# Optimization experiments

Hardware: AMD Instinct MI355X
Metric: run time of the kernel (lower is better)

The kernel has to match this reference:

```python
import jax, jax.numpy as jnp
import numpy as np

B, N, H, W = 2, 2048, 256, 256
C = 128
STATE = 256
FEAT_IN = C + 2
MID = 6  # layer_num - 2 residual blocks
OUT_DIM = 2


def setup_inputs() -> dict:
    key = jax.random.key(0)
    ks = jax.random.split(key, 8)
    s = 0.01  # matches nn.Linear init normal_(0.0, 0.01)
    features = jax.random.normal(ks[0], (B, C, H, W), jnp.float32)
    base_point = jax.random.uniform(ks[1], (B, N, 2), dtype=jnp.float32)
    adj = jax.random.uniform(ks[2], (B, N, N), dtype=jnp.float32) / N  # row-normalized-ish adjacency
    point_mask = jnp.ones((B, 1, N, 1), jnp.float32)
    w_first = jax.random.normal(ks[3], (2, FEAT_IN, STATE), jnp.float32) * s  # fc1, fc2
    b_first = jnp.zeros((2, STATE), jnp.float32)
    w_mid = jax.random.normal(ks[4], (MID, 4, STATE, STATE), jnp.float32) * s  # per block: gcn1.fc1, gcn1.fc2, gcn2.fc1, gcn2.fc2
    b_mid = jnp.zeros((MID, 4, STATE), jnp.float32)
    w_last = jax.random.normal(ks[5], (2, STATE, STATE), jnp.float32) * s
    b_last = jnp.zeros((2, STATE), jnp.float32)
    w_fc = jax.random.normal(ks[6], (STATE, OUT_DIM), jnp.float32) * s
    b_fc = jnp.zeros((OUT_DIM,), jnp.float32)
    return dict(features=features, base_point=base_point, adj=adj, point_mask=point_mask,
                w_first=w_first, b_first=b_first, w_mid=w_mid, b_mid=b_mid,
                w_last=w_last, b_last=b_last, w_fc=w_fc, b_fc=b_fc)


def _interp(feat, coords, h, w):
    # feat: [B, H*W, C]; coords: [B, N, 2] in [0,1] (x, y order as in torch code)
    Xs = coords[:, :, 0] * w
    Ys = coords[:, :, 1] * h
    X0f = jnp.floor(Xs); X1f = X0f + 1.0
    Y0f = jnp.floor(Ys); Y1f = Y0f + 1.0
    w00 = (X1f - Xs) * (Y1f - Ys)
    w01 = (X1f - Xs) * (Ys - Y0f)
    w10 = (Xs - X0f) * (Y1f - Ys)
    w11 = (Xs - X0f) * (Ys - Y0f)
    X0 = jnp.clip(X0f, 0, w - 1).astype(jnp.int32)
    X1 = jnp.clip(X1f, 0, w - 1).astype(jnp.int32)
    Y0 = jnp.clip(Y0f, 0, h - 1).astype(jnp.int32)
    Y1 = jnp.clip(Y1f, 0, h - 1).astype(jnp.int32)
    def gather(idx):  # idx: [B, N] -> [B, N, C]
        return jnp.take_along_axis(feat, idx[:, :, None], axis=1)
    m00 = gather(X0 + Y0 * w)
    m01 = gather(X0 + Y1 * w)
    m10 = gather(X1 + Y0 * w)
    m11 = gather(X1 + Y1 * w)
    return (w00[..., None] * m00 + w01[..., None] * m01 +
            w10[..., None] * m10 + w11[..., None] * m11)


def _gconv(x, adj, w1, b1, w2, b2):
    # GraphConvolution: fc1(x) + fc2(adj @ x)
    return (x @ w1 + b1) + (jnp.matmul(adj, x) @ w2 + b2)


def _res_block(x, adj, w, b):
    h = jax.nn.relu(_gconv(x, adj, w[0], b[0], w[1], b[1]))
    h = _gconv(h, adj, w[2], b[2], w[3], b[3])
    return jax.nn.relu(h + x)


def _forward(features, base_point, adj, point_mask,
             w_first, b_first, w_mid, b_mid, w_last, b_last, w_fc, b_fc):
    b, c, h, w = features.shape
    feat_flat = features.reshape(b, c, h * w).transpose(0, 2, 1)  # [B, HW, C]
    cnn_feature = _interp(feat_flat, base_point, h, w)            # [B, N, C]
    x = jnp.concatenate([cnn_feature, base_point], axis=2)        # [B, N, C+2]
    x = _gconv(x, adj, w_first[0], b_first[0], w_first[1], b_first[1])
    for i in range(MID):
        x = _res_block(x, adj, w_mid[i], b_mid[i])
    x = _gconv(x, adj, w_last[0], b_last[0], w_last[1], b_last[1])
    gcn_pred = x @ w_fc + b_fc                                    # [B, N, out_dim]
    mask = point_mask.squeeze(1)                                  # [B, N, 1]
    pred_points = base_point + gcn_pred[:, :, :2] * mask
    lap1 = base_point - jnp.matmul(adj, base_point)
    lap2 = pred_points - jnp.matmul(adj, pred_points)
    lap_energy = jnp.sqrt((((lap2 - lap1) ** 2) + 1e-10).sum(-1)).mean(-1)  # [B]
    return pred_points, gcn_pred, lap_energy


def reference(features, base_point, adj, point_mask,
              w_first, b_first, w_mid, b_mid, w_last, b_last, w_fc, b_fc):
    return _forward(features, base_point, adj, point_mask,
                    w_first, b_first, w_mid, b_mid, w_last, b_last, w_fc, b_fc)
```

## Files before the change

### kernel.cpp

```cpp
#include <hip/hip_runtime.h>
#include <hip/hip_bf16.h>
#include <math.h>

#define BB 2
#define NN 2048
#define HH 256
#define WW 256
#define CC 128
#define MIDN 6
#define YSTR 1048576

typedef __hip_bfloat16 bf16;
typedef short short8 __attribute__((ext_vector_type(8)));
typedef float f32x4 __attribute__((ext_vector_type(4)));
typedef unsigned short ushort4v __attribute__((ext_vector_type(4)));

__device__ inline float bf2f(unsigned short u) {
    return __uint_as_float(((unsigned int)u) << 16);
}
__device__ inline unsigned short f2bf_bits(float f) {
    __hip_bfloat16 h = __float2bfloat16(f);
    return *reinterpret_cast<unsigned short*>(&h);
}

__global__ void prep_kernel(const float* __restrict__ adj, bf16* __restrict__ adjB,
                            const float* __restrict__ features, const float* __restrict__ base_point,
                            bf16* __restrict__ x0p,
                            const float* __restrict__ w_first, const float* __restrict__ w_mid,
                            const float* __restrict__ w_last, bf16* __restrict__ wT) {
    __shared__ float tbuf[32][33];
    int bid = blockIdx.x;
    int t = threadIdx.x;
    if (bid < 8192) {
        int sub = bid >> 1;
        if ((bid & 1) == 0) {
            size_t i = ((size_t)sub * 256 + t) * 8;
            float4 f0 = *(const float4*)(adj + i);
            float4 f1 = *(const float4*)(adj + i + 4);
            short8 v;
            v[0] = (short)f2bf_bits(f0.x); v[1] = (short)f2bf_bits(f0.y);
            v[2] = (short)f2bf_bits(f0.z); v[3] = (short)f2bf_bits(f0.w);
            v[4] = (short)f2bf_bits(f1.x); v[5] = (short)f2bf_bits(f1.y);
            v[6] = (short)f2bf_bits(f1.z); v[7] = (short)f2bf_bits(f1.w);
            *(short8*)(adjB + i) = v;
        } else {
            int idx = sub;
            int b   = idx >> 11;
            float xs = base_point[idx * 2 + 0] * (float)WW;
            float ys = base_point[idx * 2 + 1] * (float)HH;
            float x0f = floorf(xs), y0f = floorf(ys);
            float x1f = x0f + 1.f, y1f = y0f + 1.f;
            float w00 = (x1f - xs) * (y1f - ys);
            float w01 = (x1f - xs) * (ys - y0f);
            float w10 = (xs - x0f) * (y1f - ys);
            float w11 = (xs - x0f) * (ys - y0f);
            int X0 = (int)fminf(fmaxf(x0f, 0.f), (float)(WW - 1));
            int X1 = (int)fminf(fmaxf(x1f, 0.f), (float)(WW - 1));
            int Y0 = (int)fminf(fmaxf(y0f, 0.f), (float)(HH - 1));
            int Y1 = (int)fminf(fmaxf(y1f, 0.f), (float)(HH - 1));
            int p00 = Y0 * WW + X0, p01 = Y1 * WW + X0;
            int p10 = Y0 * WW + X1, p11 = Y1 * WW + X1;
            float val = 0.f;
            if (t < CC) {
                const float* f = features + (size_t)(b * CC + t) * (HH * WW);
                val = w00 * f[p00] + w01 * f[p01] + w10 * f[p10] + w11 * f[p11];
            } else if (t == CC) {
                val = base_point[idx * 2 + 0];
            } else if (t == CC + 1) {
                val = base_point[idx * 2 + 1];
            }
            x0p[(size_t)idx * 256 + t] = __float2bfloat16(val);
        }
    } else {
        int idx = bid - 8192;
        int m   = idx >> 6;
        int sub = idx & 63;
        int bx = sub & 7, by = sub >> 3;
        const float* S; int R;
        if (m < 2)       { S = w_first + (size_t)m * 130 * 256; R = 130; }
        else if (m < 26) { S = w_mid + (size_t)(m - 2) * 65536; R = 256; }
        else             { S = w_last + (size_t)(m - 26) * 65536; R = 256; }
        bf16* D = wT + (size_t)m * 65536;
        int tx = t & 31, ty = t >> 5;
        int c0 = bx * 32, r0 = by * 32;
        #pragma unroll
        for (int k = 0; k < 4; ++k) {
            int r = r0 + ty + 8 * k;
            tbuf[ty + 8 * k][tx] = (r < R) ? S[(size_t)r * 256 + c0 + tx] : 0.f;
        }
        __syncthreads();
        #pragma unroll
        for (int k = 0; k < 4; ++k) {
            int c = c0 + ty + 8 * k;
            D[(size_t)c * 256 + r0 + tx] = __float2bfloat16(tbuf[tx][ty + 8 * k]);
        }
    }
}

__global__ __launch_bounds__(256) void s_kernel(const bf16* __restrict__ gprev,
                                                const bf16* __restrict__ Yb,
                                                const float* __restrict__ bias1,
                                                const float* __restrict__ bias2,
                                                const bf16* __restrict__ res,
                                                int relu,
                                                const bf16* __restrict__ wcat,
                                                bf16* __restrict__ xR,
                                                bf16* __restrict__ g1out,
                                                bf16* __restrict__ g2T) {
    __shared__ bf16 Al[32 * 64];
    __shared__ bf16 Bl[128 * 64];
    int tid = threadIdx.x;
    int bid = blockIdx.x;
    int lin = (bid & 7) * 64 + (bid >> 3);
    int ct = lin & 3, rt = lin >> 2;
    int lane = tid & 63, w = tid >> 6;
    int wr = w >> 1, wc = w & 1;
    int row16 = lane & 15, kg = lane >> 4;
    f32x4 acc[4] = {};
    for (int it = 0; it < 4; ++it) {
        {
            int d = tid * 16;
            int row = d >> 7;
            int cb = d & 127;
            int gcol = it * 64 + (cb >> 1);
            int ridx = rt * 32 + row;
            size_t off = (size_t)ridx * 256 + gcol;
            short8 gv = *(const short8*)(gprev + off);
            short8 pk;
            if (Yb) {
                float fv[8];
                #pragma unroll
                for (int j = 0; j < 8; ++j) fv[j] = bf2f((unsigned short)gv[j]);
                #pragma unroll
                for (int p = 0; p < 4; ++p) {
                    short8 yv = *(const short8*)(Yb + (size_t)p * YSTR + off);
                    #pragma unroll
                    for (int j = 0; j < 8; ++j) fv[j] += bf2f((unsigned short)yv[j]);
                }
                short8 rv = {};
                if (res) rv = *(const short8*)(res + off);
                #pragma unroll
                for (int j = 0; j < 8; ++j) {
                    float f = fv[j] + bias1[gcol + j] + bias2[gcol + j];
                    if (res)  f += bf2f((unsigned short)rv[j]);
                    if (relu) f = fmaxf(f, 0.f);
                    pk[j] = (short)f2bf_bits(f);
                }
            } else {
                pk = gv;
            }
            if (ct == 0) *(short8*)(xR + off) = pk;
            int byte = row * 128 + (cb ^ ((row & 7) << 4));
            *(short8*)((char*)Al + byte) = pk;
        }
        #pragma unroll
        for (int rnd = 0; rnd < 4; ++rnd) {
            int d = tid * 16 + rnd * 4096;
            int row = d >> 7;
            int cb = d & 127;
            int sc = (cb ^ ((row & 7) << 4)) >> 1;
            __builtin_amdgcn_global_load_lds(
                (const __attribute__((address_space(1))) void*)(wcat + (size_t)(ct * 128 + row) * 256 + it * 64 + sc),
                (__attribute__((address_space(3))) void*)((char*)Bl + (w << 10) + rnd * 4096),
                16, 0, 0);
        }
        asm volatile("s_waitcnt vmcnt(0)" ::: "memory");
        __syncthreads();
        #pragma unroll
        for (int kk = 0; kk < 2; ++kk) {
            int arow = wr * 16 + row16;
            int abyte = arow * 128 + (((kk * 64) + kg * 16) ^ ((arow & 7) << 4));
            short8 a = *(const short8*)((const char*)Al + abyte);
            #pragma unroll
            for (int nf = 0; nf < 4; ++nf) {
                int fr = wc * 64 + nf * 16 + row16;
                int byte = fr * 128 + (((kk * 64) + kg * 16) ^ ((fr & 7) << 4));
                short8 bfr = *(const short8*)((const char*)Bl + byte);
                acc[nf] = __builtin_amdgcn_mfma_f32_16x16x32_bf16(a, bfr, acc[nf], 0, 0, 0);
            }
        }
        __syncthreads();
    }
    int cbase = ct * 128 + wc * 64;
    int rb = rt * 32 + wr * 16 + kg * 4;
    if (cbase < 256) {
        #pragma unroll
        for (int nf = 0; nf < 4; ++nf) {
            int c = cbase + nf * 16 + row16;
            #pragma unroll
            for (int j = 0; j < 4; ++j)
                *reinterpret_cast<unsigned short*>(&g1out[(size_t)(rb + j) * 256 + c]) = f2bf_bits(acc[nf][j]);
        }
    } else {
        #pragma unroll
        for (int nf = 0; nf < 4; ++nf) {
            int c = cbase - 256 + nf * 16 + row16;
            ushort4v pk;
            #pragma unroll
            for (int j = 0; j < 4; ++j) pk[j] = f2bf_bits(acc[nf][j]);
            *(ushort4v*)(g2T + (size_t)c * 4096 + rb) = pk;
        }
    }
}

__global__ __launch_bounds__(256) void adjb_kernel(const bf16* __restrict__ adjB,
                                                   const bf16* __restrict__ g2T,
                                                   bf16* __restrict__ Ybase) {
    __shared__ bf16 Al[128 * 64];
    __shared__ bf16 Bl[64 * 64];
    int tid = threadIdx.x;
    int bid = blockIdx.x;
    int lin = (bid & 7) * 64 + (bid >> 3);
    int ct = lin & 3, rt = (lin >> 2) & 15, z = lin >> 6;
    int b = z >> 2, ks = z & 3;
    const bf16* Aadj = adjB + (size_t)b * NN * NN + (size_t)(rt * 128) * NN + ks * 512;
    const bf16* Bg   = g2T + (size_t)(ct * 64) * 4096 + b * NN + ks * 512;
    bf16* Yo = Ybase + (size_t)ks * YSTR;
    int lane = tid & 63, w = tid >> 6;
    int wr = w >> 1, wc = w & 1;
    int row16 = lane & 15, kg = lane >> 4;
    f32x4 acc[4][2] = {};
    for (int it = 0; it < 8; ++it) {
        int k0 = it * 64;
        #pragma unroll
        for (int rnd = 0; rnd < 4; ++rnd) {
            int d = tid * 16 + rnd * 4096;
            int row = d >> 7, cb = d & 127;
            int sc = (cb ^ ((row & 7) << 4)) >> 1;
            __builtin_amdgcn_global_load_lds(
                (const __attribute__((address_space(1))) void*)(Aadj + (size_t)row * NN + k0 + sc),
                (__attribute__((address_space(3))) void*)((char*)Al + (w << 10) + rnd * 4096),
                16, 0, 0);
        }
        #pragma unroll
        for (int rnd = 0; rnd < 2; ++rnd) {
            int d = tid * 16 + rnd * 4096;
            int row = d >> 7, cb = d & 127;
            int sc = (cb ^ ((row & 7) << 4)) >> 1;
            __builtin_amdgcn_global_load_lds(
                (const __attribute__((address_space(1))) void*)(Bg + (size_t)row * 4096 + k0 + sc),
                (__attribute__((address_space(3))) void*)((char*)Bl + (w << 10) + rnd * 4096),
                16, 0, 0);
        }
        asm volatile("s_waitcnt vmcnt(0)" ::: "memory");
        __syncthreads();
        #pragma unroll
        for (int kk = 0; kk < 2; ++kk) {
            short8 a[4], bfr[2];
            #pragma unroll
            for (int mf = 0; mf < 4; ++mf) {
                int row = wr * 64 + mf * 16 + row16;
                int byte = row * 128 + (((kk * 64) + kg * 16) ^ ((row & 7) << 4));
                a[mf] = *(const short8*)((const char*)Al + byte);
            }
            #pragma unroll
            for (int nf = 0; nf < 2; ++nf) {
                int fr = wc * 32 + nf * 16 + row16;
                int byte = fr * 128 + (((kk * 64) + kg * 16) ^ ((fr & 7) << 4));
                bfr[nf] = *(const short8*)((const char*)Bl + byte);
            }
            #pragma unroll
            for (int mf = 0; mf < 4; ++mf)
                #pragma unroll
                for (int nf = 0; nf < 2; ++nf)
                    acc[mf][nf] = __builtin_amdgcn_mfma_f32_16x16x32_bf16(a[mf], bfr[nf], acc[mf][nf], 0, 0, 0);
        }
        __syncthreads();
    }
    #pragma unroll
    for (int mf = 0; mf < 4; ++mf) {
        #pragma unroll
        for (int nf = 0; nf < 2; ++nf) {
            int c  = ct * 64 + wc * 32 + nf * 16 + row16;
            int r0 = b * NN + rt * 128 + wr * 64 + mf * 16 + kg * 4;
            #pragma unroll
            for (int j = 0; j < 4; ++j)
                *reinterpret_cast<unsigned short*>(&Yo[(size_t)(r0 + j) * 256 + c]) = f2bf_bits(acc[mf][nf][j]);
        }
    }
}

__global__ void head_kernel(const bf16* __restrict__ g1, const bf16* __restrict__ Yb,
                            const float* __restrict__ b_last,
                            const float* __restrict__ w_fc, const float* __restrict__ b_fc,
                            const float* __restrict__ base_point, const float* __restrict__ point_mask,
                            float* __restrict__ out, float* __restrict__ dpts) {
    int row = blockIdx.x * 256 + threadIdx.x;
    float s0 = b_fc[0], s1 = b_fc[1];
    for (int d = 0; d < 256; d += 8) {
        size_t off = (size_t)row * 256 + d;
        short8 a = *(const short8*)(g1 + off);
        float zv[8];
        #pragma unroll
        for (int j = 0; j < 8; ++j) zv[j] = bf2f((unsigned short)a[j]);
        #pragma unroll
        for (int p = 0; p < 4; ++p) {
            short8 yv = *(const short8*)(Yb + (size_t)p * YSTR + off);
            #pragma unroll
            for (int j = 0; j < 8; ++j) zv[j] += bf2f((unsigned short)yv[j]);
        }
        #pragma unroll
        for (int j = 0; j < 8; ++j) {
            float z = zv[j] + b_last[d + j] + b_last[256 + d + j];
            s0 += z * w_fc[(d + j) * 2 + 0];
            s1 += z * w_fc[(d + j) * 2 + 1];
        }
    }
    float m  = point_mask[row];
    float p0 = base_point[row * 2 + 0] + s0 * m;
    float p1 = base_point[row * 2 + 1] + s1 * m;
    out[row * 2 + 0] = p0;
    out[row * 2 + 1] = p1;
    out[2 * BB * NN + row * 2 + 0] = s0;
    out[2 * BB * NN + row * 2 + 1] = s1;
    dpts[row * 2 + 0] = s0 * m;
    dpts[row * 2 + 1] = s1 * m;
}

__global__ void lap_rows(const bf16* __restrict__ adjB, const float* __restrict__ dpts,
                         float* __restrict__ tvals) {
    int w    = threadIdx.x >> 6;
    int lane = threadIdx.x & 63;
    int row  = blockIdx.x * 4 + w;
    int b = row >> 11, n = row & 2047;
    const bf16* ar = adjB + (size_t)b * NN * NN + (size_t)n * NN;
    const float* db = dpts + (size_t)b * NN * 2;
    float s0 = 0.f, s1 = 0.f;
    for (int k4 = 0; k4 < 4; ++k4) {
        int k = k4 * 512 + lane * 8;
        short8 av = *(const short8*)(ar + k);
        #pragma unroll
        for (int j = 0; j < 8; ++j) {
            float a = bf2f((unsigned short)av[j]);
            float2 dv = *(const float2*)(db + (k + j) * 2);
            s0 += a * dv.x;
            s1 += a * dv.y;
        }
    }
    for (int off = 32; off; off >>= 1) {
        s0 += __shfl_xor(s0, off);
        s1 += __shfl_xor(s1, off);
    }
    if (lane == 0) {
        float e0 = dpts[(size_t)row * 2 + 0] - s0;
        float e1 = dpts[(size_t)row * 2 + 1] - s1;
        tvals[row] = sqrtf(e0 * e0 + e1 * e1 + 1e-10f);
    }
}

__global__ void lap_reduce(const float* __restrict__ tvals, float* __restrict__ outp) {
    __shared__ float sd[256];
    int b = blockIdx.x;
    float s = 0.f;
    for (int i = threadIdx.x; i < NN; i += 256) s += tvals[b * NN + i];
    sd[threadIdx.x] = s;
    __syncthreads();
    for (int o = 128; o; o >>= 1) {
        if (threadIdx.x < o) sd[threadIdx.x] += sd[threadIdx.x + o];
        __syncthreads();
    }
    if (threadIdx.x == 0) outp[b] = sd[0] / (float)NN;
}

extern "C" void kernel_launch(void* const* d_in, const int* in_sizes, int n_in,
                              void* d_out, int out_size, void* d_ws, size_t ws_size,
                              hipStream_t stream) {
    const float* features   = (const float*)d_in[0];
    const float* base_point = (const float*)d_in[1];
    const float* adj        = (const float*)d_in[2];
    const float* point_mask = (const float*)d_in[3];
    const float* w_first    = (const float*)d_in[4];
    const float* b_first    = (const float*)d_in[5];
    const float* w_mid      = (const float*)d_in[6];
    const float* b_mid      = (const float*)d_in[7];
    const float* w_last     = (const float*)d_in[8];
    const float* b_last     = (const float*)d_in[9];
    const float* w_fc       = (const float*)d_in[10];
    const float* b_fc       = (const float*)d_in[11];
    float* out = (float*)d_out;
    char* W = (char*)d_ws;

    bf16* adjB   = (bf16*)W;
    bf16* wT     = (bf16*)(W + 16777216);
    bf16* x0p    = (bf16*)(W + 20447232);
    bf16* g1b[2] = { (bf16*)(W + 22544384), (bf16*)(W + 24641536) };
    bf16* g2T    = (bf16*)(W + 26738688);
    bf16* Yb     = (bf16*)(W + 28835840);
    bf16* xsl[2] = { (bf16*)(W + 37224448), (bf16*)(W + 39321600) };
    bf16* xscr   = (bf16*)(W + 41418752);
    float* dpts  = (float*)(W + 43515904);
    float* tvals = (float*)(W + 43548672);

    prep_kernel<<<9984, 256, 0, stream>>>(adj, adjB, features, base_point, x0p,
                                          w_first, w_mid, w_last, wT);

    s_kernel<<<512, 256, 0, stream>>>(x0p, nullptr, nullptr, nullptr, nullptr, 0,
                                      wT, xscr, g1b[0], g2T);
    adjb_kernel<<<512, 256, 0, stream>>>(adjB, g2T, Yb);

    for (int k = 1; k < 14; ++k) {
        const float *bb1, *bb2;
        const bf16* resp = nullptr;
        bf16* xw;
        int rl;
        if (k == 1) {
            bb1 = b_first; bb2 = b_first + 256; rl = 0; xw = xsl[0];
        } else if ((k & 1) == 0) {
            int m = (k - 2) / 2;
            bb1 = b_mid + (size_t)m * 1024; bb2 = bb1 + 256;
            rl = 1; xw = xscr;
        } else {
            int m = (k - 3) / 2;
            bb1 = b_mid + (size_t)m * 1024 + 512; bb2 = bb1 + 256;
            rl = 1;
            resp = xsl[m & 1];
            xw   = xsl[((k - 1) / 2) & 1];
        }
        s_kernel<<<512, 256, 0, stream>>>(g1b[(k - 1) & 1], Yb, bb1, bb2, resp, rl,
                                          wT + (size_t)2 * k * 65536, xw, g1b[k & 1], g2T);
        adjb_kernel<<<512, 256, 0, stream>>>(adjB, g2T, Yb);
    }

    head_kernel<<<16, 256, 0, stream>>>(g1b[1], Yb, b_last, w_fc, b_fc,
                                        base_point, point_mask, out, dpts);
    lap_rows<<<1024, 256, 0, stream>>>(adjB, dpts, tvals);
    lap_reduce<<<BB, 256, 0, stream>>>(tvals, out + 4 * BB * NN);
}
```

Measured before the change: 339.9 us.

## Double-buffer LDS tiles in s_kernel and adjb_kernel, restructure prep kernel blocks

Both GEMM kernels (s_kernel and adjb_kernel) now keep two LDS buffers, so the global loads for the next k-slice are issued before the MFMAs on the current slice run. This hides memory latency, and s_kernel also overlaps the A-operand elementwise combine (bias, residual, relu). The prep kernel is reorganised: interpolation uses one wave per point with two channels per lane, and the adj conversion does 16 elements per thread, which cuts the block count from 9984 to 4864. The cost is twice the LDS per block, which may lower occupancy, plus more live registers for the prefetched A values.

```diff
diff --git a/kernel.cpp b/kernel.cpp
--- a/kernel.cpp
+++ b/kernel.cpp
@@ -31,48 +31,53 @@
     __shared__ float tbuf[32][33];
     int bid = blockIdx.x;
     int t = threadIdx.x;
-    if (bid < 8192) {
-        int sub = bid >> 1;
-        if ((bid & 1) == 0) {
-            size_t i = ((size_t)sub * 256 + t) * 8;
-            float4 f0 = *(const float4*)(adj + i);
-            float4 f1 = *(const float4*)(adj + i + 4);
+    if (bid < 1024) {
+        int wv = t >> 6, lane = t & 63;
+        int idx = bid * 4 + wv;
+        int b   = idx >> 11;
+        float bx = base_point[idx * 2 + 0];
+        float by = base_point[idx * 2 + 1];
+        float xs = bx * (float)WW;
+        float ys = by * (float)HH;
+        float x0f = floorf(xs), y0f = floorf(ys);
+        float x1f = x0f + 1.f, y1f = y0f + 1.f;
+        float w00 = (x1f - xs) * (y1f - ys);
+        float w01 = (x1f - xs) * (ys - y0f);
+        float w10 = (xs - x0f) * (y1f - ys);
+        float w11 = (xs - x0f) * (ys - y0f);
+        int X0 = (int)fminf(fmaxf(x0f, 0.f), (float)(WW - 1));
+        int X1 = (int)fminf(fmaxf(x1f, 0.f), (float)(WW - 1));
+        int Y0 = (int)fminf(fmaxf(y0f, 0.f), (float)(HH - 1));
+        int Y1 = (int)fminf(fmaxf(y1f, 0.f), (float)(HH - 1));
+        int p00 = Y0 * WW + X0, p01 = Y1 * WW + X0;
+        int p10 = Y0 * WW + X1, p11 = Y1 * WW + X1;
+        int c0 = lane * 2;
+        const float* f0 = features + (size_t)(b * CC + c0) * (HH * WW);
+        const float* f1 = f0 + HH * WW;
+        float v0 = w00 * f0[p00] + w01 * f0[p01] + w10 * f0[p10] + w11 * f0[p11];
+        float v1 = w00 * f1[p00] + w01 * f1[p01] + w10 * f1[p10] + w11 * f1[p11];
+        unsigned int pk = (unsigned int)f2bf_bits(v0) | ((unsigned int)f2bf_bits(v1) << 16);
+        *(unsigned int*)(x0p + (size_t)idx * 256 + c0) = pk;
+        unsigned int pk2 = 0;
+        if (lane == 0)
+            pk2 = (unsigned int)f2bf_bits(bx) | ((unsigned int)f2bf_bits(by) << 16);
+        *(unsigned int*)(x0p + (size_t)idx * 256 + 128 + c0) = pk2;
+    } else if (bid < 3072) {
+        int sub = bid - 1024;
+        size_t i = ((size_t)sub * 4096) + (size_t)t * 16;
+        #pragma unroll
+        for (int h = 0; h < 2; ++h) {
+            float4 f0 = *(const float4*)(adj + i + h * 8);
+            float4 f1 = *(const float4*)(adj + i + h * 8 + 4);
             short8 v;
             v[0] = (short)f2bf_bits(f0.x); v[1] = (short)f2bf_bits(f0.y);
             v[2] = (short)f2bf_bits(f0.z); v[3] = (short)f2bf_bits(f0.w);
             v[4] = (short)f2bf_bits(f1.x); v[5] = (short)f2bf_bits(f1.y);
             v[6] = (short)f2bf_bits(f1.z); v[7] = (short)f2bf_bits(f1.w);
-            *(short8*)(adjB + i) = v;
-        } else {
-            int idx = sub;
-            int b   = idx >> 11;
-            float xs = base_point[idx * 2 + 0] * (float)WW;
-            float ys = base_point[idx * 2 + 1] * (float)HH;
-            float x0f = floorf(xs), y0f = floorf(ys);
-            float x1f = x0f + 1.f, y1f = y0f + 1.f;
-            float w00 = (x1f - xs) * (y1f - ys);
-            float w01 = (x1f - xs) * (ys - y0f);
-            float w10 = (xs - x0f) * (y1f - ys);
-            float w11 = (xs - x0f) * (ys - y0f);
-            int X0 = (int)fminf(fmaxf(x0f, 0.f), (float)(WW - 1));
-            int X1 = (int)fminf(fmaxf(x1f, 0.f), (float)(WW - 1));
-            int Y0 = (int)fminf(fmaxf(y0f, 0.f), (float)(HH - 1));
-            int Y1 = (int)fminf(fmaxf(y1f, 0.f), (float)(HH - 1));
-            int p00 = Y0 * WW + X0, p01 = Y1 * WW + X0;
-            int p10 = Y0 * WW + X1, p11 = Y1 * WW + X1;
-            float val = 0.f;
-            if (t < CC) {
-                const float* f = features + (size_t)(b * CC + t) * (HH * WW);
-                val = w00 * f[p00] + w01 * f[p01] + w10 * f[p10] + w11 * f[p11];
-            } else if (t == CC) {
-                val = base_point[idx * 2 + 0];
-            } else if (t == CC + 1) {
-                val = base_point[idx * 2 + 1];
-            }
-            x0p[(size_t)idx * 256 + t] = __float2bfloat16(val);
+            *(short8*)(adjB + i + h * 8) = v;
         }
     } else {
-        int idx = bid - 8192;
+        int idx = bid - 3072;
         int m   = idx >> 6;
         int sub = idx & 63;
         int bx = sub & 7, by = sub >> 3;
@@ -107,8 +112,8 @@
                                                 bf16* __restrict__ xR,
                                                 bf16* __restrict__ g1out,
                                                 bf16* __restrict__ g2T) {
-    __shared__ bf16 Al[32 * 64];
-    __shared__ bf16 Bl[128 * 64];
+    __shared__ bf16 Al[2 * 32 * 64];
+    __shared__ bf16 Bl[2 * 128 * 64];
     int tid = threadIdx.x;
     int bid = blockIdx.x;
     int lin = (bid & 7) * 64 + (bid >> 3);
@@ -116,71 +121,98 @@
     int lane = tid & 63, w = tid >> 6;
     int wr = w >> 1, wc = w & 1;
     int row16 = lane & 15, kg = lane >> 4;
+
+    int ad  = tid * 16;
+    int arw = ad >> 7;
+    int acb = ad & 127;
+    int ridx = rt * 32 + arw;
+    int awbyte = arw * 128 + (acb ^ ((arw & 7) << 4));
+    int gc_base = acb >> 1;
+
+    #define STAGE_B(buf, it)                                                              \
+        _Pragma("unroll")                                                                 \
+        for (int rnd = 0; rnd < 4; ++rnd) {                                               \
+            int d = tid * 16 + rnd * 4096;                                                \
+            int row = d >> 7;                                                             \
+            int cb = d & 127;                                                             \
+            int sc = (cb ^ ((row & 7) << 4)) >> 1;                                        \
+            __builtin_amdgcn_global_load_lds(                                             \
+                (const __attribute__((address_space(1))) void*)(wcat + (size_t)(ct * 128 + row) * 256 + (it) * 64 + sc), \
+                (__attribute__((address_space(3))) void*)((char*)Bl + (buf) * 16384 + (w << 10) + rnd * 4096), \
+                16, 0, 0);                                                                \
+        }
+
+    short8 gv, yv0, yv1, yv2, yv3, rv;
+    #define LOADS_A(it)                                                                   \
+        {                                                                                 \
+            size_t off = (size_t)ridx * 256 + (it) * 64 + gc_base;                        \
+            gv = *(const short8*)(gprev + off);                                           \
+            if (Yb) {                                                                     \
+                yv0 = *(const short8*)(Yb + off);                                         \
+                yv1 = *(const short8*)(Yb + YSTR + off);                                  \
+                yv2 = *(const short8*)(Yb + 2 * YSTR + off);                              \
+                yv3 = *(const short8*)(Yb + 3 * YSTR + off);                              \
+                if (res) rv = *(const short8*)(res + off);                                \
+            }                                                                             \
+        }
+
+    #define COMBINE_WRITE_A(buf, it)                                                     \
+        {                                                                                 \
+            int gcol = (it) * 64 + gc_base;                                               \
+            short8 pk;                                                                    \
+            if (Yb) {                                                                     \
+                _Pragma("unroll")                                                         \
+                for (int j = 0; j < 8; ++j) {                                             \
+                    float f = bf2f((unsigned short)gv[j]) + bf2f((unsigned short)yv0[j])  \
+                            + bf2f((unsigned short)yv1[j]) + bf2f((unsigned short)yv2[j]) \
+                            + bf2f((unsigned short)yv3[j])                                \
+                            + bias1[gcol + j] + bias2[gcol + j];                          \
+                    if (res)  f += bf2f((unsigned short)rv[j]);                           \
+                    if (relu) f = fmaxf(f, 0.f);                                          \
+                    pk[j] = (short)f2bf_bits(f);                                          \
+                }                                                                         \
+            } else {                                                                      \
+                pk = gv;                                                                  \
+            }                                                                             \
+            if (ct == 0) *(short8*)(xR + (size_t)ridx * 256 + gcol) = pk;                 \
+            *(short8*)((char*)Al + (buf) * 4096 + awbyte) = pk;                           \
+        }
+
     f32x4 acc[4] = {};
+
+    STAGE_B(0, 0);
+    LOADS_A(0);
+    COMBINE_WRITE_A(0, 0);
+    asm volatile("s_waitcnt vmcnt(0) lgkmcnt(0)" ::: "memory");
+    __builtin_amdgcn_s_barrier();
+
+    #pragma unroll
     for (int it = 0; it < 4; ++it) {
-        {
-            int d = tid * 16;
-            int row = d >> 7;
-            int cb = d & 127;
-            int gcol = it * 64 + (cb >> 1);
-            int ridx = rt * 32 + row;
-            size_t off = (size_t)ridx * 256 + gcol;
-            short8 gv = *(const short8*)(gprev + off);
-            short8 pk;
-            if (Yb) {
-                float fv[8];
-                #pragma unroll
-                for (int j = 0; j < 8; ++j) fv[j] = bf2f((unsigned short)gv[j]);
-                #pragma unroll
-                for (int p = 0; p < 4; ++p) {
-                    short8 yv = *(const short8*)(Yb + (size_t)p * YSTR + off);
-                    #pragma unroll
-                    for (int j = 0; j < 8; ++j) fv[j] += bf2f((unsigned short)yv[j]);
-                }
-                short8 rv = {};
-                if (res) rv = *(const short8*)(res + off);
-                #pragma unroll
-                for (int j = 0; j < 8; ++j) {
-                    float f = fv[j] + bias1[gcol + j] + bias2[gcol + j];
-                    if (res)  f += bf2f((unsigned short)rv[j]);
-                    if (relu) f = fmaxf(f, 0.f);
-                    pk[j] = (short)f2bf_bits(f);
-                }
-            } else {
-                pk = gv;
-            }
-            if (ct == 0) *(short8*)(xR + off) = pk;
-            int byte = row * 128 + (cb ^ ((row & 7) << 4));
-            *(short8*)((char*)Al + byte) = pk;
-        }
-        #pragma unroll
-        for (int rnd = 0; rnd < 4; ++rnd) {
-            int d = tid * 16 + rnd * 4096;
-            int row = d >> 7;
-            int cb = d & 127;
-            int sc = (cb ^ ((row & 7) << 4)) >> 1;
-            __builtin_amdgcn_global_load_lds(
-                (const __attribute__((address_space(1))) void*)(wcat + (size_t)(ct * 128 + row) * 256 + it * 64 + sc),
-                (__attribute__((address_space(3))) void*)((char*)Bl + (w << 10) + rnd * 4096),
-                16, 0, 0);
-        }
-        asm volatile("s_waitcnt vmcnt(0)" ::: "memory");
-        __syncthreads();
+        int cur = it & 1;
+        if (it < 3) {
+            STAGE_B(cur ^ 1, it + 1);
+            LOADS_A(it + 1);
+        }
         #pragma unroll
         for (int kk = 0; kk < 2; ++kk) {
             int arow = wr * 16 + row16;
-            int abyte = arow * 128 + (((kk * 64) + kg * 16) ^ ((arow & 7) << 4));
+            int abyte = cur * 4096 + arow * 128 + (((kk * 64) + kg * 16) ^ ((arow & 7) << 4));
             short8 a = *(const short8*)((const char*)Al + abyte);
             #pragma unroll
             for (int nf = 0; nf < 4; ++nf) {
                 int fr = wc * 64 + nf * 16 + row16;
-                int byte = fr * 128 + (((kk * 64) + kg * 16) ^ ((fr & 7) << 4));
+                int byte = cur * 16384 + fr * 128 + (((kk * 64) + kg * 16) ^ ((fr & 7) << 4));
                 short8 bfr = *(const short8*)((const char*)Bl + byte);
                 acc[nf] = __builtin_amdgcn_mfma_f32_16x16x32_bf16(a, bfr, acc[nf], 0, 0, 0);
             }
         }
-        __syncthreads();
-    }
+        if (it < 3) {
+            COMBINE_WRITE_A(cur ^ 1, it + 1);
+            asm volatile("s_waitcnt vmcnt(0) lgkmcnt(0)" ::: "memory");
+            __builtin_amdgcn_s_barrier();
+        }
+    }
+
     int cbase = ct * 128 + wc * 64;
     int rb = rt * 32 + wr * 16 + kg * 4;
     if (cbase < 256) {
@@ -201,13 +233,16 @@
             *(ushort4v*)(g2T + (size_t)c * 4096 + rb) = pk;
         }
     }
+    #undef STAGE_B
+    #undef LOADS_A
+    #undef COMBINE_WRITE_A
 }
 
 __global__ __launch_bounds__(256) void adjb_kernel(const bf16* __restrict__ adjB,
                                                    const bf16* __restrict__ g2T,
                                                    bf16* __restrict__ Ybase) {
-    __shared__ bf16 Al[128 * 64];
-    __shared__ bf16 Bl[64 * 64];
+    __shared__ bf16 Al[2 * 128 * 64];
+    __shared__ bf16 Bl[2 * 64 * 64];
     int tid = threadIdx.x;
     int bid = blockIdx.x;
     int lin = (bid & 7) * 64 + (bid >> 3);
@@ -219,44 +254,55 @@
     int lane = tid & 63, w = tid >> 6;
     int wr = w >> 1, wc = w & 1;
     int row16 = lane & 15, kg = lane >> 4;
+
+    #define STAGE(buf, it)                                                                \
+        {                                                                                 \
+            int k0 = (it) * 64;                                                           \
+            _Pragma("unroll")                                                             \
+            for (int rnd = 0; rnd < 4; ++rnd) {                                           \
+                int d = tid * 16 + rnd * 4096;                                            \
+                int row = d >> 7, cb = d & 127;                                           \
+                int sc = (cb ^ ((row & 7) << 4)) >> 1;                                    \
+                __builtin_amdgcn_global_load_lds(                                         \
+                    (const __attribute__((address_space(1))) void*)(Aadj + (size_t)row * NN + k0 + sc), \
+                    (__attribute__((address_space(3))) void*)((char*)Al + (buf) * 16384 + (w << 10) + rnd * 4096), \
+                    16, 0, 0);                                                            \
+            }                                                                             \
+            _Pragma("unroll")                                                             \
+            for (int rnd = 0; rnd < 2; ++rnd) {                                           \
+                int d = tid * 16 + rnd * 4096;                                            \
+                int row = d >> 7, cb = d & 127;                                           \
+                int sc = (cb ^ ((row & 7) << 4)) >> 1;                                    \
+                __builtin_amdgcn_global_load_lds(                                         \
+                    (const __attribute__((address_space(1))) void*)(Bg + (size_t)row * 4096 + k0 + sc), \
+                    (__attribute__((address_space(3))) void*)((char*)Bl + (buf) * 8192 + (w << 10) + rnd * 4096), \
+                    16, 0, 0);                                                            \
+            }                                                                             \
+        }
+
     f32x4 acc[4][2] = {};
+
+    STAGE(0, 0);
+    asm volatile("s_waitcnt vmcnt(0)" ::: "memory");
+    __builtin_amdgcn_s_barrier();
+
+    #pragma unroll 1
     for (int it = 0; it < 8; ++it) {
-        int k0 = it * 64;
-        #pragma unroll
-        for (int rnd = 0; rnd < 4; ++rnd) {
-            int d = tid * 16 + rnd * 4096;
-            int row = d >> 7, cb = d & 127;
-            int sc = (cb ^ ((row & 7) << 4)) >> 1;
-            __builtin_amdgcn_global_load_lds(
-                (const __attribute__((address_space(1))) void*)(Aadj + (size_t)row * NN + k0 + sc),
-                (__attribute__((address_space(3))) void*)((char*)Al + (w << 10) + rnd * 4096),
-                16, 0, 0);
-        }
-        #pragma unroll
-        for (int rnd = 0; rnd < 2; ++rnd) {
-            int d = tid * 16 + rnd * 4096;
-            int row = d >> 7, cb = d & 127;
-            int sc = (cb ^ ((row & 7) << 4)) >> 1;
-            __builtin_amdgcn_global_load_lds(
-                (const __attribute__((address_space(1))) void*)(Bg + (size_t)row * 4096 + k0 + sc),
-                (__attribute__((address_space(3))) void*)((char*)Bl + (w << 10) + rnd * 4096),
-                16, 0, 0);
-        }
-        asm volatile("s_waitcnt vmcnt(0)" ::: "memory");
-        __syncthreads();
+        int cur = it & 1;
+        if (it < 7) STAGE(cur ^ 1, it + 1);
         #pragma unroll
         for (int kk = 0; kk < 2; ++kk) {
             short8 a[4], bfr[2];
             #pragma unroll
             for (int mf = 0; mf < 4; ++mf) {
                 int row = wr * 64 + mf * 16 + row16;
-                int byte = row * 128 + (((kk * 64) + kg * 16) ^ ((row & 7) << 4));
+                int byte = cur * 16384 + row * 128 + (((kk * 64) + kg * 16) ^ ((row & 7) << 4));
                 a[mf] = *(const short8*)((const char*)Al + byte);
             }
             #pragma unroll
             for (int nf = 0; nf < 2; ++nf) {
                 int fr = wc * 32 + nf * 16 + row16;
-                int byte = fr * 128 + (((kk * 64) + kg * 16) ^ ((fr & 7) << 4));
+                int byte = cur * 8192 + fr * 128 + (((kk * 64) + kg * 16) ^ ((fr & 7) << 4));
                 bfr[nf] = *(const short8*)((const char*)Bl + byte);
             }
             #pragma unroll
@@ -265,8 +311,10 @@
                 for (int nf = 0; nf < 2; ++nf)
                     acc[mf][nf] = __builtin_amdgcn_mfma_f32_16x16x32_bf16(a[mf], bfr[nf], acc[mf][nf], 0, 0, 0);
         }
-        __syncthreads();
-    }
+        asm volatile("s_waitcnt vmcnt(0)" ::: "memory");
+        __builtin_amdgcn_s_barrier();
+    }
+
     #pragma unroll
     for (int mf = 0; mf < 4; ++mf) {
         #pragma unroll
@@ -278,6 +326,7 @@
                 *reinterpret_cast<unsigned short*>(&Yo[(size_t)(r0 + j) * 256 + c]) = f2bf_bits(acc[mf][nf][j]);
         }
     }
+    #undef STAGE
 }
 
 __global__ void head_kernel(const bf16* __restrict__ g1, const bf16* __restrict__ Yb,
@@ -391,7 +440,7 @@
     float* dpts  = (float*)(W + 43515904);
     float* tvals = (float*)(W + 43548672);
 
-    prep_kernel<<<9984, 256, 0, stream>>>(adj, adjB, features, base_point, x0p,
+    prep_kernel<<<4864, 256, 0, stream>>>(adj, adjB, features, base_point, x0p,
                                           w_first, w_mid, w_last, wT);
 
     s_kernel<<<512, 256, 0, stream>>>(x0p, nullptr, nullptr, nullptr, nullptr, 0,
```

New measurement: 333.1 us. -2.0%, faster.
